# Kernel tuning notes

Hardware: AMD Instinct MI355X
Metric: run time of the kernel (lower is better)

Reference implementation:

```python
import jax, jax.numpy as jnp
import numpy as np

C = 256      # in_channel
C_ = C // 2  # hidden channels c_
H = 512
W = 512
EPS = 1e-5   # nn.LayerNorm default eps


def setup_inputs() -> dict:
    key = jax.random.key(0)
    ks = jax.random.split(key, 6)
    s = 0.02
    return {
        "x": jax.random.normal(ks[0], (C, H, W), jnp.float32),
        # PSA_Channel params (1x1 convs stored as dense matrices)
        "ch_cv1_w": jax.random.normal(ks[1], (C_, C), jnp.float32) * s,
        "ch_cv1_b": jnp.zeros((C_,), jnp.float32),
        "ch_cv2_w": jax.random.normal(ks[2], (1, C), jnp.float32) * s,
        "ch_cv2_b": jnp.zeros((1,), jnp.float32),
        "ch_cv3_w": jax.random.normal(ks[3], (C, C_), jnp.float32) * s,
        "ch_cv3_b": jnp.zeros((C,), jnp.float32),
        "ln_g": jnp.ones((C,), jnp.float32),
        "ln_b": jnp.zeros((C,), jnp.float32),
        # PSA_Spatial params
        "sp_cv1_w": jax.random.normal(ks[4], (C_, C), jnp.float32) * s,
        "sp_cv1_b": jnp.zeros((C_,), jnp.float32),
        "sp_cv2_w": jax.random.normal(ks[5], (C_, C), jnp.float32) * s,
        "sp_cv2_b": jnp.zeros((C_,), jnp.float32),
    }


def _conv1x1(w, b, x):
    # x: (C_in, H, W) unbatched; 1x1 conv == channel-mixing GEMM
    return jnp.einsum("oc,chw->ohw", w, x) + b[:, None, None]


def reference(x, ch_cv1_w, ch_cv1_b, ch_cv2_w, ch_cv2_b, ch_cv3_w, ch_cv3_b,
              ln_g, ln_b, sp_cv1_w, sp_cv1_b, sp_cv2_w, sp_cv2_b):
    HW = H * W

    # ---- PSA_Channel branch ----
    x1 = _conv1x1(ch_cv1_w, ch_cv1_b, x).reshape(C_, HW)            # (c_, HW)
    x2 = _conv1x1(ch_cv2_w, ch_cv2_b, x).reshape(1, HW)             # (1, HW)
    x2 = jax.nn.softmax(x2, axis=0)  # softmax over size-1 dim 0 -> ones (faithful to torch)
    # matmul broadcast: (c_,HW) @ (1,HW,1) -> (1,c_,1); then unsqueeze -> (1,c_,1,1)
    y = jnp.matmul(x1, x2[:, :, None])[..., None]
    z = jnp.einsum("oc,ncij->noij", ch_cv3_w, y) + ch_cv3_b[None, :, None, None]  # (1,C,1,1)
    # LayerNorm over normalized_shape [C,1,1]
    mu = jnp.mean(z, axis=(1, 2, 3), keepdims=True)
    var = jnp.var(z, axis=(1, 2, 3), keepdims=True)
    zn = (z - mu) * jax.lax.rsqrt(var + EPS)
    zn = zn * ln_g[None, :, None, None] + ln_b[None, :, None, None]
    ch_out = jax.nn.sigmoid(zn) * x                                 # (1,C,H,W) via broadcast

    # ---- PSA_Spatial branch ----
    s1 = _conv1x1(sp_cv1_w, sp_cv1_b, x).reshape(C_, HW)            # (c_, HW)
    s2 = jnp.mean(_conv1x1(sp_cv2_w, sp_cv2_b, x), axis=(1, 2))     # global avg pool -> (c_,)
    s2 = jax.nn.softmax(s2[:, None], axis=0)                        # (c_,1), softmax over c_
    yb = jnp.matmul(s2.T[None], s1[None])                           # (1,1,HW)
    sp_out = jax.nn.sigmoid(yb.reshape(1, H, W)) * x                # (C,H,W)

    return ch_out + sp_out                                          # (1,C,H,W)
```

## Files before the change

### kernel.cpp

```cpp
#include <hip/hip_runtime.h>
#include <math.h>

typedef float v4f __attribute__((ext_vector_type(4)));

#define C    256
#define CH   128
#define HW_  (512*512)
#define EPSV 1e-5f
#define S_SPLIT 16
#define CHUNK (HW_/S_SPLIT)

__global__ __launch_bounds__(256) void k1_partial(const float* __restrict__ x,
                                                  float* __restrict__ partials) {
    const int c = blockIdx.x, s = blockIdx.y;
    const v4f* p = (const v4f*)(x + (size_t)c * HW_ + (size_t)s * CHUNK);
    float acc = 0.f;
    #pragma unroll 4
    for (int i = threadIdx.x; i < CHUNK/4; i += 256) {
        v4f t = p[i];
        acc += t.x + t.y + t.z + t.w;
    }
    for (int off = 32; off > 0; off >>= 1) acc += __shfl_down(acc, off, 64);
    __shared__ float red[4];
    int lane = threadIdx.x & 63, wv = threadIdx.x >> 6;
    if (lane == 0) red[wv] = acc;
    __syncthreads();
    if (threadIdx.x == 0) {
        float t = red[0] + red[1] + red[2] + red[3];
        partials[c * S_SPLIT + s] = t;
    }
}

__global__ __launch_bounds__(256) void k2_small(
    const float* __restrict__ partials,
    const float* __restrict__ w1,  const float* __restrict__ b1,
    const float* __restrict__ w3,  const float* __restrict__ b3,
    const float* __restrict__ lng, const float* __restrict__ lnb,
    const float* __restrict__ sw1, const float* __restrict__ sb1,
    const float* __restrict__ sw2, const float* __restrict__ sb2,
    float* __restrict__ a_out, float* __restrict__ v_out, float* __restrict__ beff_out)
{
    __shared__ float xs[C];
    __shared__ float yv[CH];
    __shared__ float qv[CH];
    __shared__ float s2[CH];
    __shared__ float rs[4], rq[4];
    const int t = threadIdx.x;

    float sum = 0.f;
    #pragma unroll
    for (int s = 0; s < S_SPLIT; s++) sum += partials[t * S_SPLIT + s];
    xs[t] = sum;
    __syncthreads();

    if (t < CH) {
        float acc = (float)HW_ * b1[t];
        const float* wr = w1 + t * C;
        #pragma unroll 16
        for (int c = 0; c < C; c++) acc += wr[c] * xs[c];
        yv[t] = acc;
    }
    __syncthreads();

    float z = b3[t];
    {
        const float* wr = w3 + t * CH;
        #pragma unroll 16
        for (int i = 0; i < CH; i++) z += wr[i] * yv[i];
    }

    float s1v = z, sqv = z * z;
    for (int off = 32; off > 0; off >>= 1) {
        s1v += __shfl_down(s1v, off, 64);
        sqv += __shfl_down(sqv, off, 64);
    }
    int lane = t & 63, wv = t >> 6;
    if (lane == 0) { rs[wv] = s1v; rq[wv] = sqv; }
    __syncthreads();
    float ts = rs[0] + rs[1] + rs[2] + rs[3];
    float tq = rq[0] + rq[1] + rq[2] + rq[3];
    float mu  = ts / (float)C;
    float var = tq / (float)C - mu * mu;
    float zn = (z - mu) * rsqrtf(var + EPSV) * lng[t] + lnb[t];
    a_out[t] = 1.f / (1.f + expf(-zn));

    if (t < CH) {
        float acc = sb2[t];
        const float* wr = sw2 + t * C;
        const float inv = 1.f / (float)HW_;
        #pragma unroll 16
        for (int c = 0; c < C; c++) acc += wr[c] * (xs[c] * inv);
        qv[t] = acc;
    }
    __syncthreads();
    if (t < CH) {
        float m = -1e30f;
        for (int i = 0; i < CH; i++) m = fmaxf(m, qv[i]);
        float den = 0.f;
        for (int i = 0; i < CH; i++) den += expf(qv[i] - m);
        s2[t] = expf(qv[t] - m) / den;
    }
    __syncthreads();

    {
        float vv = 0.f;
        #pragma unroll 16
        for (int i = 0; i < CH; i++) vv += s2[i] * sw1[i * C + t];
        v_out[t] = vv;
    }

    if (t == 0) {
        float be = 0.f;
        for (int i = 0; i < CH; i++) be += s2[i] * sb1[i];
        *beff_out = be;
    }
}

#define TJ 64
#define K3_BLOCK 512

__global__ __launch_bounds__(K3_BLOCK) void k3_main(
    const float* __restrict__ x,
    const float* __restrict__ a, const float* __restrict__ v,
    const float* __restrict__ beff,
    float* __restrict__ out)
{
    __shared__ float tile[C][TJ];
    __shared__ float av[C];
    __shared__ float vv[C];
    __shared__ float pd[8][TJ];
    __shared__ float sj[TJ];

    const int t = threadIdx.x;
    const size_t hw0 = (size_t)blockIdx.x * TJ;

    if (t < C) { av[t] = a[t]; vv[t] = v[t]; }

    #pragma unroll
    for (int i = t; i < C*TJ/4; i += K3_BLOCK) {
        int c = i >> 4, j4 = i & 15;
        v4f val = *(const v4f*)(x + (size_t)c * HW_ + hw0 + j4 * 4);
        *(v4f*)&tile[c][j4 * 4] = val;
    }
    __syncthreads();

    {
        int j = t & 63, g = t >> 6;
        float acc = 0.f;
        #pragma unroll
        for (int cc = 0; cc < 32; cc++) {
            int c = g * 32 + cc;
            acc += vv[c] * tile[c][j];
        }
        pd[g][j] = acc;
    }
    __syncthreads();
    if (t < TJ) {
        float d = *beff;
        #pragma unroll
        for (int g = 0; g < 8; g++) d += pd[g][t];
        sj[t] = 1.f / (1.f + expf(-d));
    }
    __syncthreads();

    #pragma unroll
    for (int i = t; i < C*TJ/4; i += K3_BLOCK) {
        int c = i >> 4, j4 = i & 15;
        v4f val = *(const v4f*)&tile[c][j4 * 4];
        float ac = av[c];
        v4f o;
        o.x = (ac + sj[j4*4+0]) * val.x;
        o.y = (ac + sj[j4*4+1]) * val.y;
        o.z = (ac + sj[j4*4+2]) * val.z;
        o.w = (ac + sj[j4*4+3]) * val.w;
        __builtin_nontemporal_store(o, (v4f*)(out + (size_t)c * HW_ + hw0 + j4 * 4));
    }
}

extern "C" void kernel_launch(void* const* d_in, const int* in_sizes, int n_in,
                              void* d_out, int out_size, void* d_ws, size_t ws_size,
                              hipStream_t stream) {
    const float* x    = (const float*)d_in[0];
    const float* w1   = (const float*)d_in[1];
    const float* b1   = (const float*)d_in[2];
    const float* w3   = (const float*)d_in[5];
    const float* b3   = (const float*)d_in[6];
    const float* lng  = (const float*)d_in[7];
    const float* lnb  = (const float*)d_in[8];
    const float* sw1  = (const float*)d_in[9];
    const float* sb1  = (const float*)d_in[10];
    const float* sw2  = (const float*)d_in[11];
    const float* sb2  = (const float*)d_in[12];
    float* out = (float*)d_out;

    float* ws       = (float*)d_ws;
    float* partials = ws;
    float* a_vec    = ws + 4096;
    float* v_vec    = ws + 4096 + 256;
    float* beff     = ws + 4096 + 512;

    hipLaunchKernelGGL(k1_partial, dim3(C, S_SPLIT), dim3(256), 0, stream, x, partials);
    hipLaunchKernelGGL(k2_small, dim3(1), dim3(256), 0, stream,
                       partials, w1, b1, w3, b3, lng, lnb, sw1, sb1, sw2, sb2,
                       a_vec, v_vec, beff);
    hipLaunchKernelGGL(k3_main, dim3(HW_ / TJ), dim3(K3_BLOCK), 0, stream,
                       x, a_vec, v_vec, beff, out);
}
```

Baseline: 535.1 us.

## Fuse small parameter kernel into persistent main kernel with redundant per-block prologue

```diff
diff --git a/kernel.cpp b/kernel.cpp
--- a/kernel.cpp
+++ b/kernel.cpp
@@ -9,6 +9,10 @@
 #define EPSV 1e-5f
 #define S_SPLIT 16
 #define CHUNK (HW_/S_SPLIT)
+#define TJ   64
+#define NTILE (HW_/TJ)
+#define NBLK3 512
+#define NTHR3 512
 
 __global__ __launch_bounds__(256) void k1_partial(const float* __restrict__ x,
                                                   float* __restrict__ partials) {
@@ -31,98 +35,14 @@
     }
 }
 
-__global__ __launch_bounds__(256) void k2_small(
-    const float* __restrict__ partials,
+__global__ __launch_bounds__(NTHR3, 4) void k3_fused(
+    const float* __restrict__ x,
     const float* __restrict__ w1,  const float* __restrict__ b1,
     const float* __restrict__ w3,  const float* __restrict__ b3,
     const float* __restrict__ lng, const float* __restrict__ lnb,
     const float* __restrict__ sw1, const float* __restrict__ sb1,
     const float* __restrict__ sw2, const float* __restrict__ sb2,
-    float* __restrict__ a_out, float* __restrict__ v_out, float* __restrict__ beff_out)
-{
-    __shared__ float xs[C];
-    __shared__ float yv[CH];
-    __shared__ float qv[CH];
-    __shared__ float s2[CH];
-    __shared__ float rs[4], rq[4];
-    const int t = threadIdx.x;
-
-    float sum = 0.f;
-    #pragma unroll
-    for (int s = 0; s < S_SPLIT; s++) sum += partials[t * S_SPLIT + s];
-    xs[t] = sum;
-    __syncthreads();
-
-    if (t < CH) {
-        float acc = (float)HW_ * b1[t];
-        const float* wr = w1 + t * C;
-        #pragma unroll 16
-        for (int c = 0; c < C; c++) acc += wr[c] * xs[c];
-        yv[t] = acc;
-    }
-    __syncthreads();
-
-    float z = b3[t];
-    {
-        const float* wr = w3 + t * CH;
-        #pragma unroll 16
-        for (int i = 0; i < CH; i++) z += wr[i] * yv[i];
-    }
-
-    float s1v = z, sqv = z * z;
-    for (int off = 32; off > 0; off >>= 1) {
-        s1v += __shfl_down(s1v, off, 64);
-        sqv += __shfl_down(sqv, off, 64);
-    }
-    int lane = t & 63, wv = t >> 6;
-    if (lane == 0) { rs[wv] = s1v; rq[wv] = sqv; }
-    __syncthreads();
-    float ts = rs[0] + rs[1] + rs[2] + rs[3];
-    float tq = rq[0] + rq[1] + rq[2] + rq[3];
-    float mu  = ts / (float)C;
-    float var = tq / (float)C - mu * mu;
-    float zn = (z - mu) * rsqrtf(var + EPSV) * lng[t] + lnb[t];
-    a_out[t] = 1.f / (1.f + expf(-zn));
-
-    if (t < CH) {
-        float acc = sb2[t];
-        const float* wr = sw2 + t * C;
-        const float inv = 1.f / (float)HW_;
-        #pragma unroll 16
-        for (int c = 0; c < C; c++) acc += wr[c] * (xs[c] * inv);
-        qv[t] = acc;
-    }
-    __syncthreads();
-    if (t < CH) {
-        float m = -1e30f;
-        for (int i = 0; i < CH; i++) m = fmaxf(m, qv[i]);
-        float den = 0.f;
-        for (int i = 0; i < CH; i++) den += expf(qv[i] - m);
-        s2[t] = expf(qv[t] - m) / den;
-    }
-    __syncthreads();
-
-    {
-        float vv = 0.f;
-        #pragma unroll 16
-        for (int i = 0; i < CH; i++) vv += s2[i] * sw1[i * C + t];
-        v_out[t] = vv;
-    }
-
-    if (t == 0) {
-        float be = 0.f;
-        for (int i = 0; i < CH; i++) be += s2[i] * sb1[i];
-        *beff_out = be;
-    }
-}
-
-#define TJ 64
-#define K3_BLOCK 512
-
-__global__ __launch_bounds__(K3_BLOCK) void k3_main(
-    const float* __restrict__ x,
-    const float* __restrict__ a, const float* __restrict__ v,
-    const float* __restrict__ beff,
+    const float* __restrict__ partials,
     float* __restrict__ out)
 {
     __shared__ float tile[C][TJ];
@@ -130,50 +50,133 @@
     __shared__ float vv[C];
     __shared__ float pd[8][TJ];
     __shared__ float sj[TJ];
+    __shared__ float red1[8], red2[8];
+    __shared__ float beff_s;
 
     const int t = threadIdx.x;
-    const size_t hw0 = (size_t)blockIdx.x * TJ;
-
-    if (t < C) { av[t] = a[t]; vv[t] = v[t]; }
-
-    #pragma unroll
-    for (int i = t; i < C*TJ/4; i += K3_BLOCK) {
-        int c = i >> 4, j4 = i & 15;
-        v4f val = *(const v4f*)(x + (size_t)c * HW_ + hw0 + j4 * 4);
-        *(v4f*)&tile[c][j4 * 4] = val;
-    }
-    __syncthreads();
-
+    const int b = blockIdx.x;
+    const int lane = t & 63, wv = t >> 6;
+
+    float* xs  = &tile[0][0];
+    float* yv  = &tile[4][0];
+    float* qv  = &tile[6][0];
+    float* s2v = &tile[8][0];
+
+    if (t < C) {
+        float sum = 0.f;
+        #pragma unroll
+        for (int si = 0; si < S_SPLIT; si++) sum += partials[t * S_SPLIT + si];
+        xs[t] = sum;
+    }
+    __syncthreads();
+
+    if (t < CH) {
+        float acc = (float)HW_ * b1[t];
+        const float* wr = w1 + t * C;
+        #pragma unroll 16
+        for (int c = 0; c < C; c++) acc += wr[c] * xs[c];
+        yv[t] = acc;
+
+        float q = 0.f;
+        const float* wq = sw2 + t * C;
+        #pragma unroll 16
+        for (int c = 0; c < C; c++) q += wq[c] * xs[c];
+        qv[t] = fmaf(q, 1.f / (float)HW_, sb2[t]);
+    }
+    __syncthreads();
+
+    float z = 0.f;
+    if (t < C) {
+        z = b3[t];
+        const float* wr = w3 + t * CH;
+        #pragma unroll 16
+        for (int i = 0; i < CH; i++) z += wr[i] * yv[i];
+    }
+    float s1v = z, sqv = z * z;
+    for (int off = 32; off > 0; off >>= 1) {
+        s1v += __shfl_down(s1v, off, 64);
+        sqv += __shfl_down(sqv, off, 64);
+    }
+    if (lane == 0) { red1[wv] = s1v; red2[wv] = sqv; }
+    __syncthreads();
     {
-        int j = t & 63, g = t >> 6;
+        float ts = 0.f, tq = 0.f;
+        #pragma unroll
+        for (int w = 0; w < 8; w++) { ts += red1[w]; tq += red2[w]; }
+        if (t < C) {
+            float mu  = ts / (float)C;
+            float var = tq / (float)C - mu * mu;
+            float zn  = (z - mu) * rsqrtf(var + EPSV) * lng[t] + lnb[t];
+            av[t] = 1.f / (1.f + expf(-zn));
+        }
+    }
+
+    if (t < CH) {
+        float m = -1e30f;
+        for (int i = 0; i < CH; i++) m = fmaxf(m, qv[i]);
+        float den = 0.f;
+        for (int i = 0; i < CH; i++) den += expf(qv[i] - m);
+        s2v[t] = expf(qv[t] - m) / den;
+    }
+    __syncthreads();
+
+    if (t < C) {
         float acc = 0.f;
-        #pragma unroll
-        for (int cc = 0; cc < 32; cc++) {
-            int c = g * 32 + cc;
-            acc += vv[c] * tile[c][j];
-        }
-        pd[g][j] = acc;
-    }
-    __syncthreads();
-    if (t < TJ) {
-        float d = *beff;
-        #pragma unroll
-        for (int g = 0; g < 8; g++) d += pd[g][t];
-        sj[t] = 1.f / (1.f + expf(-d));
-    }
-    __syncthreads();
-
-    #pragma unroll
-    for (int i = t; i < C*TJ/4; i += K3_BLOCK) {
-        int c = i >> 4, j4 = i & 15;
-        v4f val = *(const v4f*)&tile[c][j4 * 4];
-        float ac = av[c];
-        v4f o;
-        o.x = (ac + sj[j4*4+0]) * val.x;
-        o.y = (ac + sj[j4*4+1]) * val.y;
-        o.z = (ac + sj[j4*4+2]) * val.z;
-        o.w = (ac + sj[j4*4+3]) * val.w;
-        __builtin_nontemporal_store(o, (v4f*)(out + (size_t)c * HW_ + hw0 + j4 * 4));
+        #pragma unroll 16
+        for (int i = 0; i < CH; i++) acc += s2v[i] * sw1[i * C + t];
+        vv[t] = acc;
+    }
+    if (wv == 0) {
+        float be = 0.f;
+        for (int i = lane; i < CH; i += 64) be += s2v[i] * sb1[i];
+        for (int off = 32; off > 0; off >>= 1) be += __shfl_down(be, off, 64);
+        if (lane == 0) beff_s = be;
+    }
+    __syncthreads();
+
+    for (int tileIdx = b; tileIdx < NTILE; tileIdx += NBLK3) {
+        const size_t hw0 = (size_t)tileIdx * TJ;
+
+        #pragma unroll
+        for (int i = t; i < C * TJ / 4; i += NTHR3) {
+            int c = i >> 4, j4 = i & 15;
+            v4f val = *(const v4f*)(x + (size_t)c * HW_ + hw0 + j4 * 4);
+            *(v4f*)&tile[c][j4 * 4] = val;
+        }
+        __syncthreads();
+
+        {
+            int j = t & 63, g = t >> 6;
+            float acc = 0.f;
+            #pragma unroll
+            for (int cc = 0; cc < 32; cc++) {
+                int c = g * 32 + cc;
+                acc += vv[c] * tile[c][j];
+            }
+            pd[g][j] = acc;
+        }
+        __syncthreads();
+        if (t < TJ) {
+            float d = beff_s;
+            #pragma unroll
+            for (int g = 0; g < 8; g++) d += pd[g][t];
+            sj[t] = 1.f / (1.f + expf(-d));
+        }
+        __syncthreads();
+
+        #pragma unroll
+        for (int i = t; i < C * TJ / 4; i += NTHR3) {
+            int c = i >> 4, j4 = i & 15;
+            v4f val = *(const v4f*)&tile[c][j4 * 4];
+            float ac = av[c];
+            v4f o;
+            o.x = (ac + sj[j4 * 4 + 0]) * val.x;
+            o.y = (ac + sj[j4 * 4 + 1]) * val.y;
+            o.z = (ac + sj[j4 * 4 + 2]) * val.z;
+            o.w = (ac + sj[j4 * 4 + 3]) * val.w;
+            __builtin_nontemporal_store(o, (v4f*)(out + (size_t)c * HW_ + hw0 + j4 * 4));
+        }
+        __syncthreads();
     }
 }
 
@@ -192,17 +195,10 @@
     const float* sw2  = (const float*)d_in[11];
     const float* sb2  = (const float*)d_in[12];
     float* out = (float*)d_out;
-
-    float* ws       = (float*)d_ws;
-    float* partials = ws;
-    float* a_vec    = ws + 4096;
-    float* v_vec    = ws + 4096 + 256;
-    float* beff     = ws + 4096 + 512;
+    float* partials = (float*)d_ws;
 
     hipLaunchKernelGGL(k1_partial, dim3(C, S_SPLIT), dim3(256), 0, stream, x, partials);
-    hipLaunchKernelGGL(k2_small, dim3(1), dim3(256), 0, stream,
-                       partials, w1, b1, w3, b3, lng, lnb, sw1, sb1, sw2, sb2,
-                       a_vec, v_vec, beff);
-    hipLaunchKernelGGL(k3_main, dim3(HW_ / TJ), dim3(K3_BLOCK), 0, stream,
-                       x, a_vec, v_vec, beff, out);
+    hipLaunchKernelGGL(k3_fused, dim3(NBLK3), dim3(NTHR3), 0, stream,
+                       x, w1, b1, w3, b3, lng, lnb, sw1, sb1, sw2, sb2,
+                       partials, out);
 }
```

Result: no change. 540.9 us (+1.1%).
